# Kernel tuning notes

Measured on AMD Instinct MI355X. Metric: run time of the kernel, lower is better.

## Reference

```python
import jax, jax.numpy as jnp
import numpy as np

G = 128        # number of graphs
N = 512        # nodes per graph
F_IN = 128     # n_feat
H = 128        # agg_hidden
L = 5          # n_layer
FC = 128       # fc_hidden
C = 10         # n_class
E_HALF = 8192  # undirected edge pairs per graph (symmetrized -> 16384 directed)


def setup_inputs() -> dict:
    key = jax.random.key(0)
    ks = jax.random.split(key, 8)
    x = jax.random.normal(ks[0], (G * N, F_IN), dtype=jnp.float32)
    # per-graph random edges, offset into the block-diagonal node index space
    s = jax.random.randint(ks[1], (G, E_HALF), 0, N)
    d = jax.random.randint(ks[2], (G, E_HALF), 0, N)
    off = (jnp.arange(G) * N)[:, None]
    s = (s + off).reshape(-1)
    d = (d + off).reshape(-1)
    src = jnp.concatenate([s, d])  # symmetric adjacency (edges + reversed)
    dst = jnp.concatenate([d, s])
    eps = jnp.zeros((L,), jnp.float32)  # nn.Parameter(torch.zeros(n_layer))
    W = jax.random.normal(ks[3], (L, H, H), jnp.float32) / jnp.sqrt(H)
    b = jnp.zeros((L, H), jnp.float32)
    fc1_w = jax.random.normal(ks[4], (H, FC), jnp.float32) / jnp.sqrt(H)
    fc1_b = jnp.zeros((FC,), jnp.float32)
    fc2_w = jax.random.normal(ks[5], (FC, C), jnp.float32) / jnp.sqrt(FC)
    fc2_b = jnp.zeros((C,), jnp.float32)
    return {"x": x, "eps": eps, "W": W, "b": b,
            "fc1_w": fc1_w, "fc1_b": fc1_b, "fc2_w": fc2_w, "fc2_b": fc2_b,
            "src": src, "dst": dst}


def reference(x, eps, W, b, fc1_w, fc1_b, fc2_w, fc2_b, src, dst):
    n = x.shape[0]
    h = x
    for i in range(L):
        # sparse Adj @ h : gather along src, scatter-add to dst
        pooled = jax.ops.segment_sum(h[src], dst, num_segments=n)
        h = jax.nn.relu(((1.0 + eps[i]) * h + pooled) @ W[i] + b[i])
        # dropout p=0.0 / eval mode -> identity
    hg = h.reshape(G, N, -1).sum(axis=1)          # sum readout over nodes
    hg = jax.nn.relu(hg @ fc1_w + fc1_b)
    return jax.nn.softmax(hg @ fc2_w + fc2_b, axis=-1)
```

## Files before the change

### kernel.cpp

```cpp
#include <hip/hip_runtime.h>

#define NODES 65536
#define GNUM  128
#define NPG   512
#define FDIM  128

#define OFF_A   0u
#define OFF_WT  (16u<<20)
#define OFF_HTA (17u<<20)
#define OFF_HTB (33u<<20)

typedef short bf16x8 __attribute__((ext_vector_type(8)));
typedef float f32x4  __attribute__((ext_vector_type(4)));
typedef unsigned short u16;

#define GLB_AS __attribute__((address_space(1)))
#define LDS_AS __attribute__((address_space(3)))

static __device__ inline void gload16(const void* g, void* l) {
    __builtin_amdgcn_global_load_lds((const GLB_AS unsigned*)g,
                                     (LDS_AS unsigned*)l, 16, 0, 0);
}

static __device__ inline unsigned bf1(float x) {
    unsigned b = __float_as_uint(x);
    return (b + 0x7fffu + ((b >> 16) & 1u)) >> 16;
}
static __device__ inline unsigned pack_bf2(float x, float y) {
    return bf1(x) | (bf1(y) << 16);
}
static __device__ inline bf16x8 cvt8n(unsigned x) {
    union { bf16x8 v; unsigned u[4]; } r;
#pragma unroll
    for (int i = 0; i < 4; ++i) {
        float f0 = (float)((x >> (8 * i)) & 0xFu);
        float f1 = (float)((x >> (8 * i + 4)) & 0xFu);
        r.u[i] = (__float_as_uint(f0) >> 16) | (__float_as_uint(f1) & 0xffff0000u);
    }
    return r.v;
}

__global__ __launch_bounds__(256) void k_cvtT(const float* __restrict__ x,
                                              u16* __restrict__ hT) {
    __shared__ char Cs[128 * 144];
    int t = threadIdx.x;
    int m0 = blockIdx.x * 64;
    int g = m0 >> 9, ml0 = m0 & 511;
#pragma unroll
    for (int it = 0; it < 8; ++it) {
        int i = t + 256 * it;
        int nl = i >> 5, fq = i & 31;
        float4 v = *(const float4*)(x + (size_t)(m0 + nl) * FDIM + fq * 4);
        *(u16*)(Cs + (fq * 4 + 0) * 144 + nl * 2) = (u16)bf1(v.x);
        *(u16*)(Cs + (fq * 4 + 1) * 144 + nl * 2) = (u16)bf1(v.y);
        *(u16*)(Cs + (fq * 4 + 2) * 144 + nl * 2) = (u16)bf1(v.z);
        *(u16*)(Cs + (fq * 4 + 3) * 144 + nl * 2) = (u16)bf1(v.w);
    }
    __syncthreads();
    u16* hg = hT + (size_t)g * 65536 + ml0;
#pragma unroll
    for (int j = 0; j < 4; ++j) {
        int idx = t + 256 * j;
        int f = idx >> 3, piece = idx & 7;
        uint4 v = *(const uint4*)(Cs + f * 144 + piece * 16);
        *(uint4*)((char*)(hg + (size_t)f * 512) + piece * 16) = v;
    }
}

__global__ __launch_bounds__(256) void k_wt(const float* __restrict__ W,
                                            u16* __restrict__ wt) {
    int idx = blockIdx.x * 256 + threadIdx.x;
    int l = idx >> 14, r = idx & 16383;
    int n = r >> 7, k = r & 127;
    wt[idx] = (u16)bf1(W[(l << 14) + k * 128 + n]);
}

__global__ __launch_bounds__(1024) void k_adense(const int* __restrict__ src,
                                                 const int* __restrict__ dst,
                                                 unsigned* __restrict__ A4,
                                                 int halfE) {
    __shared__ uint4 cnt4[512 * 16];
    unsigned* cnt = (unsigned*)cnt4;
    int g = blockIdx.x;
    int t = threadIdx.x;
#pragma unroll
    for (int j = 0; j < 8; ++j) cnt4[t + 1024 * j] = make_uint4(0u, 0u, 0u, 0u);
    __syncthreads();
    int epg = halfE / GNUM;
#pragma unroll
    for (int r = 0; r < 2; ++r) {
        int base = r * halfE + g * epg;
        const int4* s4 = (const int4*)(src + base);
        const int4* d4 = (const int4*)(dst + base);
#pragma unroll
        for (int it = 0; it < 2; ++it) {
            int i = t + 1024 * it;
            int4 sv = s4[i], dv = d4[i];
            int s, d;
            s = sv.x & 511; d = dv.x & 511; atomicAdd(&cnt[d * 64 + (s >> 3)], 1u << ((s & 7) * 4));
            s = sv.y & 511; d = dv.y & 511; atomicAdd(&cnt[d * 64 + (s >> 3)], 1u << ((s & 7) * 4));
            s = sv.z & 511; d = dv.z & 511; atomicAdd(&cnt[d * 64 + (s >> 3)], 1u << ((s & 7) * 4));
            s = sv.w & 511; d = dv.w & 511; atomicAdd(&cnt[d * 64 + (s >> 3)], 1u << ((s & 7) * 4));
        }
    }
    __syncthreads();
    uint4* Ao = (uint4*)(A4 + (size_t)g * 512 * 64);
#pragma unroll
    for (int j = 0; j < 8; ++j) Ao[t + 1024 * j] = cnt4[t + 1024 * j];
}

__global__ __launch_bounds__(256, 2) void k_layer(const u16* __restrict__ hT,
                                                  u16* __restrict__ hTo,
                                                  const unsigned char* __restrict__ A,
                                                  const u16* __restrict__ wt,
                                                  const float* __restrict__ bias,
                                                  const float* __restrict__ eps) {
    __shared__ uint4 smem16[75776 / 16];
    char* smem = (char*)smem16;
    char* Ps = smem + 40960;
    int t = threadIdx.x;
    int w = t >> 6, lane = t & 63;
    int q = lane >> 4, ln = lane & 15;
    int g = blockIdx.x & 127, dq = blockIdx.x >> 7;
    const unsigned char* Ab = A + (size_t)g * (512 * 256) + (size_t)dq * 128 * 256;
    const u16* hb = hT + (size_t)g * 65536;

    int pA = t;
    int rowA = pA >> 1;
    const unsigned char* gA = Ab + rowA * 256 + (pA & 1) * 16;
    f32x4 acc[2][8];
#pragma unroll
    for (int mt = 0; mt < 2; ++mt)
#pragma unroll
        for (int nt = 0; nt < 8; ++nt) acc[mt][nt] = (f32x4){0.f, 0.f, 0.f, 0.f};

    gload16(gA, smem + pA * 16);
#pragma unroll
    for (int j = 0; j < 4; ++j) {
        int p = t + 256 * j; int f = p >> 3;
        gload16((const char*)hb + (size_t)f * 1024 + (((p & 7) ^ (f & 7)) << 4),
                smem + 8192 + p * 16);
    }
    __syncthreads();
    int rA0 = w * 32 + ln;
    for (int ch = 0; ch < 8; ++ch) {
        char* Asc = smem + (ch & 1) * 4096;
        char* Bsc = smem + 8192 + (ch & 1) * 16384;
        if (ch < 7) {
            char* Asn = smem + ((ch + 1) & 1) * 4096;
            char* Bsn = smem + 8192 + ((ch + 1) & 1) * 16384;
            gload16(gA + (ch + 1) * 32, Asn + pA * 16);
#pragma unroll
            for (int j = 0; j < 4; ++j) {
                int p = t + 256 * j; int f = p >> 3;
                gload16((const char*)hb + (size_t)f * 1024 + (ch + 1) * 128
                            + (((p & 7) ^ (f & 7)) << 4),
                        Bsn + p * 16);
            }
        }
#pragma unroll
        for (int kcL = 0; kcL < 2; ++kcL) {
            bf16x8 af0 = cvt8n(*(const unsigned*)(Asc + rA0 * 32 + kcL * 16 + q * 4));
            bf16x8 af1 = cvt8n(*(const unsigned*)(Asc + (rA0 + 16) * 32 + kcL * 16 + q * 4));
#pragma unroll
            for (int nt = 0; nt < 8; ++nt) {
                int f = nt * 16 + ln;
                int sB = f * 8 + ((kcL * 4 + q) ^ (f & 7));
                bf16x8 bf = *(const bf16x8*)(Bsc + sB * 16);
                acc[0][nt] = __builtin_amdgcn_mfma_f32_16x16x32_bf16(af0, bf, acc[0][nt], 0, 0, 0);
                acc[1][nt] = __builtin_amdgcn_mfma_f32_16x16x32_bf16(af1, bf, acc[1][nt], 0, 0, 0);
            }
        }
        __syncthreads();
    }
    float ep = 1.f + eps[0];
#pragma unroll
    for (int mt = 0; mt < 2; ++mt) {
        int rl0 = w * 32 + mt * 16 + q * 4;
        int mb0 = dq * 128 + rl0;
#pragma unroll
        for (int nt = 0; nt < 8; ++nt) {
            int f = nt * 16 + ln;
            uint2 sv = *(const uint2*)(hb + (size_t)f * 512 + mb0);
            float s0 = __uint_as_float(sv.x << 16);
            float s1 = __uint_as_float(sv.x & 0xffff0000u);
            float s2 = __uint_as_float(sv.y << 16);
            float s3 = __uint_as_float(sv.y & 0xffff0000u);
            f32x4 a = acc[mt][nt];
            *(u16*)(Ps + (rl0 + 0) * 272 + f * 2) = (u16)bf1(fmaf(ep, s0, a[0]));
            *(u16*)(Ps + (rl0 + 1) * 272 + f * 2) = (u16)bf1(fmaf(ep, s1, a[1]));
            *(u16*)(Ps + (rl0 + 2) * 272 + f * 2) = (u16)bf1(fmaf(ep, s2, a[2]));
            *(u16*)(Ps + (rl0 + 3) * 272 + f * 2) = (u16)bf1(fmaf(ep, s3, a[3]));
        }
    }
    __syncthreads();
    f32x4 acc2[2][8];
#pragma unroll
    for (int mt = 0; mt < 2; ++mt)
#pragma unroll
        for (int nt = 0; nt < 8; ++nt) acc2[mt][nt] = (f32x4){0.f, 0.f, 0.f, 0.f};
#pragma unroll
    for (int ks = 0; ks < 4; ++ks) {
        bf16x8 af0 = *(const bf16x8*)(Ps + rA0 * 272 + ks * 64 + q * 16);
        bf16x8 af1 = *(const bf16x8*)(Ps + (rA0 + 16) * 272 + ks * 64 + q * 16);
#pragma unroll
        for (int nt = 0; nt < 8; ++nt) {
            bf16x8 bf = *(const bf16x8*)(wt + (size_t)(nt * 16 + ln) * 128 + ks * 32 + q * 8);
            acc2[0][nt] = __builtin_amdgcn_mfma_f32_16x16x32_bf16(af0, bf, acc2[0][nt], 0, 0, 0);
            acc2[1][nt] = __builtin_amdgcn_mfma_f32_16x16x32_bf16(af1, bf, acc2[1][nt], 0, 0, 0);
        }
    }
    __syncthreads();
#pragma unroll
    for (int mt = 0; mt < 2; ++mt) {
        int rl0 = w * 32 + mt * 16 + q * 4;
#pragma unroll
        for (int nt = 0; nt < 8; ++nt) {
            int n = nt * 16 + ln;
            float bv = bias[n];
            f32x4 a = acc2[mt][nt];
            *(uint2*)(Ps + n * 272 + rl0 * 2) =
                make_uint2(pack_bf2(fmaxf(a[0] + bv, 0.f), fmaxf(a[1] + bv, 0.f)),
                           pack_bf2(fmaxf(a[2] + bv, 0.f), fmaxf(a[3] + bv, 0.f)));
        }
    }
    __syncthreads();
    u16* ho = hTo + (size_t)g * 65536 + dq * 128;
#pragma unroll
    for (int j = 0; j < 8; ++j) {
        int idx = t + 256 * j;
        int f = idx >> 4, piece = idx & 15;
        uint4 v = *(const uint4*)(Ps + f * 272 + piece * 16);
        *(uint4*)((char*)(ho + (size_t)f * 512) + piece * 16) = v;
    }
}

__global__ __launch_bounds__(128) void k_r(const u16* __restrict__ hT,
                                           const float* __restrict__ fc1w,
                                           const float* __restrict__ fc1b,
                                           const float* __restrict__ fc2w,
                                           const float* __restrict__ fc2b,
                                           float* __restrict__ out) {
    __shared__ float hg[128], z[128], lg[10];
    int g = blockIdx.x, t = threadIdx.x;
    const uint4* row = (const uint4*)(hT + (size_t)g * 65536 + (size_t)t * 512);
    float acc = 0.f;
#pragma unroll 4
    for (int i = 0; i < 64; ++i) {
        uint4 u = row[i];
        acc += __uint_as_float(u.x << 16) + __uint_as_float(u.x & 0xffff0000u);
        acc += __uint_as_float(u.y << 16) + __uint_as_float(u.y & 0xffff0000u);
        acc += __uint_as_float(u.z << 16) + __uint_as_float(u.z & 0xffff0000u);
        acc += __uint_as_float(u.w << 16) + __uint_as_float(u.w & 0xffff0000u);
    }
    hg[t] = acc;
    __syncthreads();
    float a1 = fc1b[t];
#pragma unroll 4
    for (int k = 0; k < 128; ++k) a1 = fmaf(hg[k], fc1w[k * 128 + t], a1);
    z[t] = fmaxf(a1, 0.f);
    __syncthreads();
    if (t < 10) {
        float l2 = fc2b[t];
        for (int k = 0; k < 128; ++k) l2 = fmaf(z[k], fc2w[k * 10 + t], l2);
        lg[t] = l2;
    }
    __syncthreads();
    if (t < 10) {
        float m = lg[0];
        for (int c = 1; c < 10; ++c) m = fmaxf(m, lg[c]);
        float ssum = 0.f;
        for (int c = 0; c < 10; ++c) ssum += expf(lg[c] - m);
        out[g * 10 + t] = expf(lg[t] - m) / ssum;
    }
}

extern "C" void kernel_launch(void* const* d_in, const int* in_sizes, int n_in,
                              void* d_out, int out_size, void* d_ws, size_t ws_size,
                              hipStream_t stream) {
    const float* x    = (const float*)d_in[0];
    const float* eps  = (const float*)d_in[1];
    const float* W    = (const float*)d_in[2];
    const float* b    = (const float*)d_in[3];
    const float* fc1w = (const float*)d_in[4];
    const float* fc1b = (const float*)d_in[5];
    const float* fc2w = (const float*)d_in[6];
    const float* fc2b = (const float*)d_in[7];
    const int*   src  = (const int*)d_in[8];
    const int*   dst  = (const int*)d_in[9];
    int E = in_sizes[8];
    int halfE = E >> 1;

    char* ws  = (char*)d_ws;
    unsigned char* Abuf = (unsigned char*)(ws + OFF_A);
    u16*  wtb = (u16*)(ws + OFF_WT);
    u16*  hta = (u16*)(ws + OFF_HTA);
    u16*  htb = (u16*)(ws + OFF_HTB);
    float* out = (float*)d_out;

    k_cvtT<<<NODES / 64, 256, 0, stream>>>(x, hta);
    k_wt<<<5 * 128 * 128 / 256, 256, 0, stream>>>(W, wtb);
    k_adense<<<GNUM, 1024, 0, stream>>>(src, dst, (unsigned*)Abuf, halfE);

    u16* cur = hta;
    u16* nxt = htb;
    for (int l = 0; l < 5; ++l) {
        k_layer<<<GNUM * 4, 256, 0, stream>>>(cur, nxt, Abuf,
                                              wtb + l * 128 * 128, b + l * 128, eps + l);
        u16* tmp = cur; cur = nxt; nxt = tmp;
    }
    k_r<<<GNUM, 128, 0, stream>>>(cur, fc1w, fc1b, fc2w, fc2b, out);
}
```

Measured before the change: 251.0 us.

## Triple-buffer adjacency and feature tiles with explicit vmcnt waits in layer kernel

Converts the double-buffered k-loop in the layer kernel into a three-stage ring buffer that prefetches two chunks ahead. It replaces __syncthreads with manual s_waitcnt vmcnt counts plus raw barriers, so that more global-to-LDS loads stay in flight while the MFMAs run. The output staging buffer now overlaps the ring buffer, which lowers total LDS use. The hand-set vmcnt values rely on an exact count of outstanding loads per thread, so a wrong count would cause data races.

```diff
diff --git a/kernel.cpp b/kernel.cpp
--- a/kernel.cpp
+++ b/kernel.cpp
@@ -115,9 +115,9 @@
                                                   const u16* __restrict__ wt,
                                                   const float* __restrict__ bias,
                                                   const float* __restrict__ eps) {
-    __shared__ uint4 smem16[75776 / 16];
+    __shared__ uint4 smem16[61440 / 16];
     char* smem = (char*)smem16;
-    char* Ps = smem + 40960;
+    char* Ps = smem + 12288;
     int t = threadIdx.x;
     int w = t >> 6, lane = t & 63;
     int q = lane >> 4, ln = lane & 15;
@@ -126,38 +126,46 @@
     const u16* hb = hT + (size_t)g * 65536;
 
     int pA = t;
-    int rowA = pA >> 1;
-    const unsigned char* gA = Ab + rowA * 256 + (pA & 1) * 16;
+    const unsigned char* gA = Ab + (pA >> 1) * 256 + (pA & 1) * 16;
     f32x4 acc[2][8];
 #pragma unroll
     for (int mt = 0; mt < 2; ++mt)
 #pragma unroll
         for (int nt = 0; nt < 8; ++nt) acc[mt][nt] = (f32x4){0.f, 0.f, 0.f, 0.f};
 
-    gload16(gA, smem + pA * 16);
-#pragma unroll
-    for (int j = 0; j < 4; ++j) {
-        int p = t + 256 * j; int f = p >> 3;
-        gload16((const char*)hb + (size_t)f * 1024 + (((p & 7) ^ (f & 7)) << 4),
-                smem + 8192 + p * 16);
-    }
-    __syncthreads();
+#pragma unroll
+    for (int c = 0; c < 2; ++c) {
+        gload16(gA + c * 32, smem + c * 4096 + pA * 16);
+#pragma unroll
+        for (int j = 0; j < 4; ++j) {
+            int p = t + 256 * j; int f = p >> 3;
+            gload16((const char*)hb + (size_t)f * 1024 + c * 128
+                        + (((p & 7) ^ (f & 7)) << 4),
+                    smem + 12288 + c * 16384 + p * 16);
+        }
+    }
     int rA0 = w * 32 + ln;
+#pragma unroll
     for (int ch = 0; ch < 8; ++ch) {
-        char* Asc = smem + (ch & 1) * 4096;
-        char* Bsc = smem + 8192 + (ch & 1) * 16384;
-        if (ch < 7) {
-            char* Asn = smem + ((ch + 1) & 1) * 4096;
-            char* Bsn = smem + 8192 + ((ch + 1) & 1) * 16384;
-            gload16(gA + (ch + 1) * 32, Asn + pA * 16);
+        char* Asc = smem + (ch % 3) * 4096;
+        char* Bsc = smem + 12288 + (ch % 3) * 16384;
+        if (ch + 2 < 8) {
+            int cn = ch + 2;
+            char* Asn = smem + (cn % 3) * 4096;
+            char* Bsn = smem + 12288 + (cn % 3) * 16384;
+            gload16(gA + cn * 32, Asn + pA * 16);
 #pragma unroll
             for (int j = 0; j < 4; ++j) {
                 int p = t + 256 * j; int f = p >> 3;
-                gload16((const char*)hb + (size_t)f * 1024 + (ch + 1) * 128
+                gload16((const char*)hb + (size_t)f * 1024 + cn * 128
                             + (((p & 7) ^ (f & 7)) << 4),
                         Bsn + p * 16);
             }
         }
+        if (ch < 6)      asm volatile("s_waitcnt vmcnt(10)" ::: "memory");
+        else if (ch < 7) asm volatile("s_waitcnt vmcnt(5)" ::: "memory");
+        else             asm volatile("s_waitcnt vmcnt(0)" ::: "memory");
+        __builtin_amdgcn_s_barrier();
 #pragma unroll
         for (int kcL = 0; kcL < 2; ++kcL) {
             bf16x8 af0 = cvt8n(*(const unsigned*)(Asc + rA0 * 32 + kcL * 16 + q * 4));
@@ -171,7 +179,7 @@
                 acc[1][nt] = __builtin_amdgcn_mfma_f32_16x16x32_bf16(af1, bf, acc[1][nt], 0, 0, 0);
             }
         }
-        __syncthreads();
+        __builtin_amdgcn_s_barrier();
     }
     float ep = 1.f + eps[0];
 #pragma unroll
```

After: 245.6 us. 2.1% less time.

## Fuse all GIN layers and readout into one persistent per-graph kernel

Applied to the files above, without the earlier changes.

Replaces the five per-layer launches and the readout launch with a single kernel that runs one 1024-thread block per graph. Each block keeps the graph's transposed bf16 node features resident in 128 KB of LDS across all layers, so they no longer round-trip through global memory between layers. The dense-W matmul is serialized over four quarters of the nodes to fit in LDS scratch. The readout and MLP run in the same kernel, and the x and W conversion kernels are merged into one launch. The trade-off is only 128 blocks (one per graph, one block per CU), plus quarter-serialized phases with many barriers, which may underuse the GPU compared with 512 blocks per layer.

```diff
diff --git a/kernel.cpp b/kernel.cpp
--- a/kernel.cpp
+++ b/kernel.cpp
@@ -1,6 +1,5 @@
 #include <hip/hip_runtime.h>
 
-#define NODES 65536
 #define GNUM  128
 #define NPG   512
 #define FDIM  128
@@ -8,7 +7,6 @@
 #define OFF_A   0u
 #define OFF_WT  (16u<<20)
 #define OFF_HTA (17u<<20)
-#define OFF_HTB (33u<<20)
 
 typedef short bf16x8 __attribute__((ext_vector_type(8)));
 typedef float f32x4  __attribute__((ext_vector_type(4)));
@@ -40,11 +38,21 @@
     return r.v;
 }
 
-__global__ __launch_bounds__(256) void k_cvtT(const float* __restrict__ x,
-                                              u16* __restrict__ hT) {
+__global__ __launch_bounds__(256) void k_prep(const float* __restrict__ x,
+                                              u16* __restrict__ hT,
+                                              const float* __restrict__ W,
+                                              u16* __restrict__ wt) {
     __shared__ char Cs[128 * 144];
     int t = threadIdx.x;
-    int m0 = blockIdx.x * 64;
+    int bid = blockIdx.x;
+    if (bid >= 1024) {
+        int idx = (bid - 1024) * 256 + t;
+        int l = idx >> 14, r = idx & 16383;
+        int n = r >> 7, k = r & 127;
+        wt[idx] = (u16)bf1(W[(l << 14) + k * 128 + n]);
+        return;
+    }
+    int m0 = bid * 64;
     int g = m0 >> 9, ml0 = m0 & 511;
 #pragma unroll
     for (int it = 0; it < 8; ++it) {
@@ -65,14 +73,6 @@
         uint4 v = *(const uint4*)(Cs + f * 144 + piece * 16);
         *(uint4*)((char*)(hg + (size_t)f * 512) + piece * 16) = v;
     }
-}
-
-__global__ __launch_bounds__(256) void k_wt(const float* __restrict__ W,
-                                            u16* __restrict__ wt) {
-    int idx = blockIdx.x * 256 + threadIdx.x;
-    int l = idx >> 14, r = idx & 16383;
-    int n = r >> 7, k = r & 127;
-    wt[idx] = (u16)bf1(W[(l << 14) + k * 128 + n]);
 }
 
 __global__ __launch_bounds__(1024) void k_adense(const int* __restrict__ src,
@@ -109,160 +109,162 @@
     for (int j = 0; j < 8; ++j) Ao[t + 1024 * j] = cnt4[t + 1024 * j];
 }
 
-__global__ __launch_bounds__(256, 2) void k_layer(const u16* __restrict__ hT,
-                                                  u16* __restrict__ hTo,
-                                                  const unsigned char* __restrict__ A,
-                                                  const u16* __restrict__ wt,
-                                                  const float* __restrict__ bias,
-                                                  const float* __restrict__ eps) {
-    __shared__ uint4 smem16[75776 / 16];
-    char* smem = (char*)smem16;
-    char* Ps = smem + 40960;
+__global__ __launch_bounds__(1024) void k_gin(
+        const u16* __restrict__ hT,
+        const unsigned char* __restrict__ A,
+        const u16* __restrict__ wt,
+        const float* __restrict__ bias,
+        const float* __restrict__ eps,
+        const float* __restrict__ fc1w, const float* __restrict__ fc1b,
+        const float* __restrict__ fc2w, const float* __restrict__ fc2b,
+        float* __restrict__ out) {
+    __shared__ uint4 smem16[163840 / 16];
+    char* hTl = (char*)smem16;
+    char* scr = (char*)smem16 + 131072;
     int t = threadIdx.x;
     int w = t >> 6, lane = t & 63;
     int q = lane >> 4, ln = lane & 15;
-    int g = blockIdx.x & 127, dq = blockIdx.x >> 7;
-    const unsigned char* Ab = A + (size_t)g * (512 * 256) + (size_t)dq * 128 * 256;
-    const u16* hb = hT + (size_t)g * 65536;
-
-    int pA = t;
-    int rowA = pA >> 1;
-    const unsigned char* gA = Ab + rowA * 256 + (pA & 1) * 16;
-    f32x4 acc[2][8];
-#pragma unroll
-    for (int mt = 0; mt < 2; ++mt)
-#pragma unroll
-        for (int nt = 0; nt < 8; ++nt) acc[mt][nt] = (f32x4){0.f, 0.f, 0.f, 0.f};
-
-    gload16(gA, smem + pA * 16);
-#pragma unroll
-    for (int j = 0; j < 4; ++j) {
-        int p = t + 256 * j; int f = p >> 3;
-        gload16((const char*)hb + (size_t)f * 1024 + (((p & 7) ^ (f & 7)) << 4),
-                smem + 8192 + p * 16);
-    }
-    __syncthreads();
+    int g = blockIdx.x;
+    const unsigned char* Ab = A + (size_t)g * 131072;
+    const u16* hgb = hT + (size_t)g * 65536;
     int rA0 = w * 32 + ln;
-    for (int ch = 0; ch < 8; ++ch) {
-        char* Asc = smem + (ch & 1) * 4096;
-        char* Bsc = smem + 8192 + (ch & 1) * 16384;
-        if (ch < 7) {
-            char* Asn = smem + ((ch + 1) & 1) * 4096;
-            char* Bsn = smem + 8192 + ((ch + 1) & 1) * 16384;
-            gload16(gA + (ch + 1) * 32, Asn + pA * 16);
-#pragma unroll
-            for (int j = 0; j < 4; ++j) {
-                int p = t + 256 * j; int f = p >> 3;
-                gload16((const char*)hb + (size_t)f * 1024 + (ch + 1) * 128
-                            + (((p & 7) ^ (f & 7)) << 4),
-                        Bsn + p * 16);
+
+#pragma unroll
+    for (int j = 0; j < 8; ++j) {
+        int p = t + 1024 * j;
+        int f = p >> 6, bb = p & 63;
+        gload16((const char*)hgb + (size_t)f * 1024 + ((bb ^ (f & 7)) << 4),
+                hTl + p * 16);
+    }
+    const unsigned char* gA = Ab + (t >> 1) * 256 + (t & 1) * 16;
+
+    for (int l = 0; l < 5; ++l) {
+        const u16* wl = wt + l * 16384;
+        float ep = 1.f + eps[l];
+        gload16(gA, scr + t * 16);
+        f32x4 acc[2][8];
+#pragma unroll
+        for (int mt = 0; mt < 2; ++mt)
+#pragma unroll
+            for (int nt = 0; nt < 8; ++nt) acc[mt][nt] = (f32x4){0.f, 0.f, 0.f, 0.f};
+#pragma unroll
+        for (int ch = 0; ch < 8; ++ch) {
+            char* Asc = scr + (ch & 1) * 16384;
+            if (ch < 7) {
+                gload16(gA + (ch + 1) * 32, scr + ((ch + 1) & 1) * 16384 + t * 16);
+                asm volatile("s_waitcnt vmcnt(1)" ::: "memory");
+            } else {
+                asm volatile("s_waitcnt vmcnt(0)" ::: "memory");
             }
+            __builtin_amdgcn_s_barrier();
+#pragma unroll
+            for (int kcL = 0; kcL < 2; ++kcL) {
+                bf16x8 af0 = cvt8n(*(const unsigned*)(Asc + rA0 * 32 + kcL * 16 + q * 4));
+                bf16x8 af1 = cvt8n(*(const unsigned*)(Asc + (rA0 + 16) * 32 + kcL * 16 + q * 4));
+#pragma unroll
+                for (int nt = 0; nt < 8; ++nt) {
+                    int f = nt * 16 + ln;
+                    int bb = (ch * 8 + ((kcL * 4 + q) ^ (f & 7))) << 4;
+                    bf16x8 bf = *(const bf16x8*)(hTl + f * 1024 + bb);
+                    acc[0][nt] = __builtin_amdgcn_mfma_f32_16x16x32_bf16(af0, bf, acc[0][nt], 0, 0, 0);
+                    acc[1][nt] = __builtin_amdgcn_mfma_f32_16x16x32_bf16(af1, bf, acc[1][nt], 0, 0, 0);
+                }
+            }
+            __builtin_amdgcn_s_barrier();
         }
-#pragma unroll
-        for (int kcL = 0; kcL < 2; ++kcL) {
-            bf16x8 af0 = cvt8n(*(const unsigned*)(Asc + rA0 * 32 + kcL * 16 + q * 4));
-            bf16x8 af1 = cvt8n(*(const unsigned*)(Asc + (rA0 + 16) * 32 + kcL * 16 + q * 4));
-#pragma unroll
-            for (int nt = 0; nt < 8; ++nt) {
-                int f = nt * 16 + ln;
-                int sB = f * 8 + ((kcL * 4 + q) ^ (f & 7));
-                bf16x8 bf = *(const bf16x8*)(Bsc + sB * 16);
-                acc[0][nt] = __builtin_amdgcn_mfma_f32_16x16x32_bf16(af0, bf, acc[0][nt], 0, 0, 0);
-                acc[1][nt] = __builtin_amdgcn_mfma_f32_16x16x32_bf16(af1, bf, acc[1][nt], 0, 0, 0);
+        for (int qp = 0; qp < 4; ++qp) {
+            if ((w >> 2) == qp) {
+#pragma unroll
+                for (int mt = 0; mt < 2; ++mt) {
+                    int rl0 = (w & 3) * 32 + mt * 16 + q * 4;
+                    int node0 = qp * 128 + rl0;
+#pragma unroll
+                    for (int nt = 0; nt < 8; ++nt) {
+                        int f = nt * 16 + ln;
+                        const char* sp = hTl + f * 1024
+                            + (((node0 >> 3) ^ (f & 7)) << 4) + (node0 & 7) * 2;
+                        uint2 sv = *(const uint2*)sp;
+                        float s0 = __uint_as_float(sv.x << 16);
+                        float s1 = __uint_as_float(sv.x & 0xffff0000u);
+                        float s2 = __uint_as_float(sv.y << 16);
+                        float s3 = __uint_as_float(sv.y & 0xffff0000u);
+                        f32x4 a = acc[mt][nt];
+                        int r0 = rl0 + 0, r1 = rl0 + 1, r2 = rl0 + 2, r3 = rl0 + 3;
+                        *(u16*)(scr + r0 * 256 + ((f * 2) ^ ((r0 & 7) << 4))) = (u16)bf1(fmaf(ep, s0, a[0]));
+                        *(u16*)(scr + r1 * 256 + ((f * 2) ^ ((r1 & 7) << 4))) = (u16)bf1(fmaf(ep, s1, a[1]));
+                        *(u16*)(scr + r2 * 256 + ((f * 2) ^ ((r2 & 7) << 4))) = (u16)bf1(fmaf(ep, s2, a[2]));
+                        *(u16*)(scr + r3 * 256 + ((f * 2) ^ ((r3 & 7) << 4))) = (u16)bf1(fmaf(ep, s3, a[3]));
+                    }
+                }
             }
+            __syncthreads();
+            if ((w >> 2) == qp) {
+                f32x4 acc2[2][8];
+#pragma unroll
+                for (int mt = 0; mt < 2; ++mt)
+#pragma unroll
+                    for (int nt = 0; nt < 8; ++nt) acc2[mt][nt] = (f32x4){0.f, 0.f, 0.f, 0.f};
+                int r0 = (w & 3) * 32 + ln;
+                int xr = (r0 & 7) << 4;
+#pragma unroll
+                for (int ks = 0; ks < 4; ++ks) {
+                    bf16x8 af0 = *(const bf16x8*)(scr + r0 * 256 + ((ks * 64 + q * 16) ^ xr));
+                    bf16x8 af1 = *(const bf16x8*)(scr + (r0 + 16) * 256 + ((ks * 64 + q * 16) ^ xr));
+#pragma unroll
+                    for (int nt = 0; nt < 8; ++nt) {
+                        bf16x8 bf = *(const bf16x8*)(wl + (size_t)(nt * 16 + ln) * 128 + ks * 32 + q * 8);
+                        acc2[0][nt] = __builtin_amdgcn_mfma_f32_16x16x32_bf16(af0, bf, acc2[0][nt], 0, 0, 0);
+                        acc2[1][nt] = __builtin_amdgcn_mfma_f32_16x16x32_bf16(af1, bf, acc2[1][nt], 0, 0, 0);
+                    }
+                }
+#pragma unroll
+                for (int mt = 0; mt < 2; ++mt) {
+                    int rl0 = (w & 3) * 32 + mt * 16 + q * 4;
+                    int node0 = qp * 128 + rl0;
+#pragma unroll
+                    for (int nt = 0; nt < 8; ++nt) {
+                        int n = nt * 16 + ln;
+                        float bv = bias[l * 128 + n];
+                        f32x4 a = acc2[mt][nt];
+                        char* op = hTl + n * 1024
+                            + (((node0 >> 3) ^ (n & 7)) << 4) + (node0 & 7) * 2;
+                        *(uint2*)op =
+                            make_uint2(pack_bf2(fmaxf(a[0] + bv, 0.f), fmaxf(a[1] + bv, 0.f)),
+                                       pack_bf2(fmaxf(a[2] + bv, 0.f), fmaxf(a[3] + bv, 0.f)));
+                    }
+                }
+            }
+            __syncthreads();
         }
-        __syncthreads();
-    }
-    float ep = 1.f + eps[0];
-#pragma unroll
-    for (int mt = 0; mt < 2; ++mt) {
-        int rl0 = w * 32 + mt * 16 + q * 4;
-        int mb0 = dq * 128 + rl0;
-#pragma unroll
-        for (int nt = 0; nt < 8; ++nt) {
-            int f = nt * 16 + ln;
-            uint2 sv = *(const uint2*)(hb + (size_t)f * 512 + mb0);
-            float s0 = __uint_as_float(sv.x << 16);
-            float s1 = __uint_as_float(sv.x & 0xffff0000u);
-            float s2 = __uint_as_float(sv.y << 16);
-            float s3 = __uint_as_float(sv.y & 0xffff0000u);
-            f32x4 a = acc[mt][nt];
-            *(u16*)(Ps + (rl0 + 0) * 272 + f * 2) = (u16)bf1(fmaf(ep, s0, a[0]));
-            *(u16*)(Ps + (rl0 + 1) * 272 + f * 2) = (u16)bf1(fmaf(ep, s1, a[1]));
-            *(u16*)(Ps + (rl0 + 2) * 272 + f * 2) = (u16)bf1(fmaf(ep, s2, a[2]));
-            *(u16*)(Ps + (rl0 + 3) * 272 + f * 2) = (u16)bf1(fmaf(ep, s3, a[3]));
+    }
+    float* hg = (float*)scr;
+    float* zz = hg + 128;
+    float* lg = zz + 128;
+    if (t < 128) {
+        float acc = 0.f;
+        const char* row = hTl + (size_t)t * 1024;
+#pragma unroll 4
+        for (int i = 0; i < 64; ++i) {
+            int bb = (i + (t & 63)) & 63;
+            uint4 u = *(const uint4*)(row + bb * 16);
+            acc += __uint_as_float(u.x << 16) + __uint_as_float(u.x & 0xffff0000u);
+            acc += __uint_as_float(u.y << 16) + __uint_as_float(u.y & 0xffff0000u);
+            acc += __uint_as_float(u.z << 16) + __uint_as_float(u.z & 0xffff0000u);
+            acc += __uint_as_float(u.w << 16) + __uint_as_float(u.w & 0xffff0000u);
         }
-    }
-    __syncthreads();
-    f32x4 acc2[2][8];
-#pragma unroll
-    for (int mt = 0; mt < 2; ++mt)
-#pragma unroll
-        for (int nt = 0; nt < 8; ++nt) acc2[mt][nt] = (f32x4){0.f, 0.f, 0.f, 0.f};
-#pragma unroll
-    for (int ks = 0; ks < 4; ++ks) {
-        bf16x8 af0 = *(const bf16x8*)(Ps + rA0 * 272 + ks * 64 + q * 16);
-        bf16x8 af1 = *(const bf16x8*)(Ps + (rA0 + 16) * 272 + ks * 64 + q * 16);
-#pragma unroll
-        for (int nt = 0; nt < 8; ++nt) {
-            bf16x8 bf = *(const bf16x8*)(wt + (size_t)(nt * 16 + ln) * 128 + ks * 32 + q * 8);
-            acc2[0][nt] = __builtin_amdgcn_mfma_f32_16x16x32_bf16(af0, bf, acc2[0][nt], 0, 0, 0);
-            acc2[1][nt] = __builtin_amdgcn_mfma_f32_16x16x32_bf16(af1, bf, acc2[1][nt], 0, 0, 0);
-        }
-    }
-    __syncthreads();
-#pragma unroll
-    for (int mt = 0; mt < 2; ++mt) {
-        int rl0 = w * 32 + mt * 16 + q * 4;
-#pragma unroll
-        for (int nt = 0; nt < 8; ++nt) {
-            int n = nt * 16 + ln;
-            float bv = bias[n];
-            f32x4 a = acc2[mt][nt];
-            *(uint2*)(Ps + n * 272 + rl0 * 2) =
-                make_uint2(pack_bf2(fmaxf(a[0] + bv, 0.f), fmaxf(a[1] + bv, 0.f)),
-                           pack_bf2(fmaxf(a[2] + bv, 0.f), fmaxf(a[3] + bv, 0.f)));
-        }
-    }
-    __syncthreads();
-    u16* ho = hTo + (size_t)g * 65536 + dq * 128;
-#pragma unroll
-    for (int j = 0; j < 8; ++j) {
-        int idx = t + 256 * j;
-        int f = idx >> 4, piece = idx & 15;
-        uint4 v = *(const uint4*)(Ps + f * 272 + piece * 16);
-        *(uint4*)((char*)(ho + (size_t)f * 512) + piece * 16) = v;
-    }
-}
-
-__global__ __launch_bounds__(128) void k_r(const u16* __restrict__ hT,
-                                           const float* __restrict__ fc1w,
-                                           const float* __restrict__ fc1b,
-                                           const float* __restrict__ fc2w,
-                                           const float* __restrict__ fc2b,
-                                           float* __restrict__ out) {
-    __shared__ float hg[128], z[128], lg[10];
-    int g = blockIdx.x, t = threadIdx.x;
-    const uint4* row = (const uint4*)(hT + (size_t)g * 65536 + (size_t)t * 512);
-    float acc = 0.f;
+        hg[t] = acc;
+    }
+    __syncthreads();
+    if (t < 128) {
+        float a1 = fc1b[t];
 #pragma unroll 4
-    for (int i = 0; i < 64; ++i) {
-        uint4 u = row[i];
-        acc += __uint_as_float(u.x << 16) + __uint_as_float(u.x & 0xffff0000u);
-        acc += __uint_as_float(u.y << 16) + __uint_as_float(u.y & 0xffff0000u);
-        acc += __uint_as_float(u.z << 16) + __uint_as_float(u.z & 0xffff0000u);
-        acc += __uint_as_float(u.w << 16) + __uint_as_float(u.w & 0xffff0000u);
-    }
-    hg[t] = acc;
-    __syncthreads();
-    float a1 = fc1b[t];
-#pragma unroll 4
-    for (int k = 0; k < 128; ++k) a1 = fmaf(hg[k], fc1w[k * 128 + t], a1);
-    z[t] = fmaxf(a1, 0.f);
+        for (int k = 0; k < 128; ++k) a1 = fmaf(hg[k], fc1w[k * 128 + t], a1);
+        zz[t] = fmaxf(a1, 0.f);
+    }
     __syncthreads();
     if (t < 10) {
         float l2 = fc2b[t];
-        for (int k = 0; k < 128; ++k) l2 = fmaf(z[k], fc2w[k * 10 + t], l2);
+        for (int k = 0; k < 128; ++k) l2 = fmaf(zz[k], fc2w[k * 10 + t], l2);
         lg[t] = l2;
     }
     __syncthreads();
@@ -295,19 +297,10 @@
     unsigned char* Abuf = (unsigned char*)(ws + OFF_A);
     u16*  wtb = (u16*)(ws + OFF_WT);
     u16*  hta = (u16*)(ws + OFF_HTA);
-    u16*  htb = (u16*)(ws + OFF_HTB);
     float* out = (float*)d_out;
 
-    k_cvtT<<<NODES / 64, 256, 0, stream>>>(x, hta);
-    k_wt<<<5 * 128 * 128 / 256, 256, 0, stream>>>(W, wtb);
+    k_prep<<<1344, 256, 0, stream>>>(x, hta, W, wtb);
     k_adense<<<GNUM, 1024, 0, stream>>>(src, dst, (unsigned*)Abuf, halfE);
-
-    u16* cur = hta;
-    u16* nxt = htb;
-    for (int l = 0; l < 5; ++l) {
-        k_layer<<<GNUM * 4, 256, 0, stream>>>(cur, nxt, Abuf,
-                                              wtb + l * 128 * 128, b + l * 128, eps + l);
-        u16* tmp = cur; cur = nxt; nxt = tmp;
-    }
-    k_r<<<GNUM, 128, 0, stream>>>(cur, fc1w, fc1b, fc2w, fc2b, out);
-}
+    k_gin<<<GNUM, 1024, 0, stream>>>(hta, Abuf, wtb, b, eps,
+                                     fc1w, fc1b, fc2w, fc2b, out);
+}
```

New measurement: 869.2 us. 3.46x slower.

## Split layer kernel into 64-row blocks, hold adjacency in registers, fuse prep kernels

Applied to the files above, without the earlier changes.

Each layer block now covers 64 destination rows instead of 128, so the grid doubles to 1024 blocks. The four waves are split as 2 row halves by 2 feature halves. The adjacency tile is preloaded into registers rather than staged through LDS, which shrinks shared memory from about 74KB to 32KB and allows 4 blocks per CU. The per-chunk sync becomes an explicit vmcnt wait plus barrier. The feature transpose and weight transpose kernels are merged into one launch. In exchange, every block now loads the full 128-feature h slab for only half as many output rows, doubling that traffic, and register pressure rises from the 32-entry adjacency array.

```diff
diff --git a/kernel.cpp b/kernel.cpp
--- a/kernel.cpp
+++ b/kernel.cpp
@@ -1,6 +1,5 @@
 #include <hip/hip_runtime.h>
 
-#define NODES 65536
 #define GNUM  128
 #define NPG   512
 #define FDIM  128
@@ -40,11 +39,21 @@
     return r.v;
 }
 
-__global__ __launch_bounds__(256) void k_cvtT(const float* __restrict__ x,
-                                              u16* __restrict__ hT) {
+__global__ __launch_bounds__(256) void k_prep(const float* __restrict__ x,
+                                              u16* __restrict__ hT,
+                                              const float* __restrict__ W,
+                                              u16* __restrict__ wt) {
     __shared__ char Cs[128 * 144];
     int t = threadIdx.x;
-    int m0 = blockIdx.x * 64;
+    int bid = blockIdx.x;
+    if (bid >= 1024) {
+        int idx = (bid - 1024) * 256 + t;
+        int l = idx >> 14, r = idx & 16383;
+        int n = r >> 7, k = r & 127;
+        wt[idx] = (u16)bf1(W[(l << 14) + k * 128 + n]);
+        return;
+    }
+    int m0 = bid * 64;
     int g = m0 >> 9, ml0 = m0 & 511;
 #pragma unroll
     for (int it = 0; it < 8; ++it) {
@@ -67,14 +76,6 @@
     }
 }
 
-__global__ __launch_bounds__(256) void k_wt(const float* __restrict__ W,
-                                            u16* __restrict__ wt) {
-    int idx = blockIdx.x * 256 + threadIdx.x;
-    int l = idx >> 14, r = idx & 16383;
-    int n = r >> 7, k = r & 127;
-    wt[idx] = (u16)bf1(W[(l << 14) + k * 128 + n]);
-}
-
 __global__ __launch_bounds__(1024) void k_adense(const int* __restrict__ src,
                                                  const int* __restrict__ dst,
                                                  unsigned* __restrict__ A4,
@@ -109,47 +110,51 @@
     for (int j = 0; j < 8; ++j) Ao[t + 1024 * j] = cnt4[t + 1024 * j];
 }
 
-__global__ __launch_bounds__(256, 2) void k_layer(const u16* __restrict__ hT,
+__global__ __launch_bounds__(256, 4) void k_layer(const u16* __restrict__ hT,
                                                   u16* __restrict__ hTo,
                                                   const unsigned char* __restrict__ A,
                                                   const u16* __restrict__ wt,
                                                   const float* __restrict__ bias,
                                                   const float* __restrict__ eps) {
-    __shared__ uint4 smem16[75776 / 16];
+    __shared__ uint4 smem16[32768 / 16];
     char* smem = (char*)smem16;
-    char* Ps = smem + 40960;
+    char* Ps = smem;
     int t = threadIdx.x;
     int w = t >> 6, lane = t & 63;
     int q = lane >> 4, ln = lane & 15;
     int g = blockIdx.x & 127, dq = blockIdx.x >> 7;
-    const unsigned char* Ab = A + (size_t)g * (512 * 256) + (size_t)dq * 128 * 256;
+    const unsigned char* Ab = A + (size_t)g * 131072 + (size_t)dq * 64 * 256;
     const u16* hb = hT + (size_t)g * 65536;
-
-    int pA = t;
-    int rowA = pA >> 1;
-    const unsigned char* gA = Ab + rowA * 256 + (pA & 1) * 16;
-    f32x4 acc[2][8];
+    int rA0 = (w & 1) * 32 + ln;
+    int fh0 = (w >> 1) * 64;
+
+    unsigned aA[32];
+#pragma unroll
+    for (int ch = 0; ch < 8; ++ch)
+#pragma unroll
+        for (int kcL = 0; kcL < 2; ++kcL)
+#pragma unroll
+            for (int h = 0; h < 2; ++h)
+                aA[ch * 4 + kcL * 2 + h] = *(const unsigned*)
+                    (Ab + (size_t)(rA0 + h * 16) * 256 + ch * 32 + kcL * 16 + q * 4);
+
+    f32x4 acc[2][4];
 #pragma unroll
     for (int mt = 0; mt < 2; ++mt)
 #pragma unroll
-        for (int nt = 0; nt < 8; ++nt) acc[mt][nt] = (f32x4){0.f, 0.f, 0.f, 0.f};
-
-    gload16(gA, smem + pA * 16);
+        for (int nt = 0; nt < 4; ++nt) acc[mt][nt] = (f32x4){0.f, 0.f, 0.f, 0.f};
+
 #pragma unroll
     for (int j = 0; j < 4; ++j) {
         int p = t + 256 * j; int f = p >> 3;
         gload16((const char*)hb + (size_t)f * 1024 + (((p & 7) ^ (f & 7)) << 4),
-                smem + 8192 + p * 16);
-    }
-    __syncthreads();
-    int rA0 = w * 32 + ln;
+                smem + p * 16);
+    }
+#pragma unroll
     for (int ch = 0; ch < 8; ++ch) {
-        char* Asc = smem + (ch & 1) * 4096;
-        char* Bsc = smem + 8192 + (ch & 1) * 16384;
+        char* Bsc = smem + (ch & 1) * 16384;
         if (ch < 7) {
-            char* Asn = smem + ((ch + 1) & 1) * 4096;
-            char* Bsn = smem + 8192 + ((ch + 1) & 1) * 16384;
-            gload16(gA + (ch + 1) * 32, Asn + pA * 16);
+            char* Bsn = smem + ((ch + 1) & 1) * 16384;
 #pragma unroll
             for (int j = 0; j < 4; ++j) {
                 int p = t + 256 * j; int f = p >> 3;
@@ -157,30 +162,34 @@
                             + (((p & 7) ^ (f & 7)) << 4),
                         Bsn + p * 16);
             }
-        }
+            asm volatile("s_waitcnt vmcnt(4)" ::: "memory");
+        } else {
+            asm volatile("s_waitcnt vmcnt(0)" ::: "memory");
+        }
+        __builtin_amdgcn_s_barrier();
 #pragma unroll
         for (int kcL = 0; kcL < 2; ++kcL) {
-            bf16x8 af0 = cvt8n(*(const unsigned*)(Asc + rA0 * 32 + kcL * 16 + q * 4));
-            bf16x8 af1 = cvt8n(*(const unsigned*)(Asc + (rA0 + 16) * 32 + kcL * 16 + q * 4));
-#pragma unroll
-            for (int nt = 0; nt < 8; ++nt) {
-                int f = nt * 16 + ln;
+            bf16x8 af0 = cvt8n(aA[ch * 4 + kcL * 2 + 0]);
+            bf16x8 af1 = cvt8n(aA[ch * 4 + kcL * 2 + 1]);
+#pragma unroll
+            for (int nt = 0; nt < 4; ++nt) {
+                int f = fh0 + nt * 16 + ln;
                 int sB = f * 8 + ((kcL * 4 + q) ^ (f & 7));
                 bf16x8 bf = *(const bf16x8*)(Bsc + sB * 16);
                 acc[0][nt] = __builtin_amdgcn_mfma_f32_16x16x32_bf16(af0, bf, acc[0][nt], 0, 0, 0);
                 acc[1][nt] = __builtin_amdgcn_mfma_f32_16x16x32_bf16(af1, bf, acc[1][nt], 0, 0, 0);
             }
         }
-        __syncthreads();
+        __builtin_amdgcn_s_barrier();
     }
     float ep = 1.f + eps[0];
 #pragma unroll
     for (int mt = 0; mt < 2; ++mt) {
-        int rl0 = w * 32 + mt * 16 + q * 4;
-        int mb0 = dq * 128 + rl0;
-#pragma unroll
-        for (int nt = 0; nt < 8; ++nt) {
-            int f = nt * 16 + ln;
+        int rl0 = (w & 1) * 32 + mt * 16 + q * 4;
+        int mb0 = dq * 64 + rl0;
+#pragma unroll
+        for (int nt = 0; nt < 4; ++nt) {
+            int f = fh0 + nt * 16 + ln;
             uint2 sv = *(const uint2*)(hb + (size_t)f * 512 + mb0);
             float s0 = __uint_as_float(sv.x << 16);
             float s1 = __uint_as_float(sv.x & 0xffff0000u);
@@ -194,18 +203,19 @@
         }
     }
     __syncthreads();
-    f32x4 acc2[2][8];
+    f32x4 acc2[2][4];
 #pragma unroll
     for (int mt = 0; mt < 2; ++mt)
 #pragma unroll
-        for (int nt = 0; nt < 8; ++nt) acc2[mt][nt] = (f32x4){0.f, 0.f, 0.f, 0.f};
+        for (int nt = 0; nt < 4; ++nt) acc2[mt][nt] = (f32x4){0.f, 0.f, 0.f, 0.f};
 #pragma unroll
     for (int ks = 0; ks < 4; ++ks) {
         bf16x8 af0 = *(const bf16x8*)(Ps + rA0 * 272 + ks * 64 + q * 16);
         bf16x8 af1 = *(const bf16x8*)(Ps + (rA0 + 16) * 272 + ks * 64 + q * 16);
 #pragma unroll
-        for (int nt = 0; nt < 8; ++nt) {
-            bf16x8 bf = *(const bf16x8*)(wt + (size_t)(nt * 16 + ln) * 128 + ks * 32 + q * 8);
+        for (int nt = 0; nt < 4; ++nt) {
+            int n = fh0 + nt * 16 + ln;
+            bf16x8 bf = *(const bf16x8*)(wt + (size_t)n * 128 + ks * 32 + q * 8);
             acc2[0][nt] = __builtin_amdgcn_mfma_f32_16x16x32_bf16(af0, bf, acc2[0][nt], 0, 0, 0);
             acc2[1][nt] = __builtin_amdgcn_mfma_f32_16x16x32_bf16(af1, bf, acc2[1][nt], 0, 0, 0);
         }
@@ -213,24 +223,24 @@
     __syncthreads();
 #pragma unroll
     for (int mt = 0; mt < 2; ++mt) {
-        int rl0 = w * 32 + mt * 16 + q * 4;
-#pragma unroll
-        for (int nt = 0; nt < 8; ++nt) {
-            int n = nt * 16 + ln;
+        int rl0 = (w & 1) * 32 + mt * 16 + q * 4;
+#pragma unroll
+        for (int nt = 0; nt < 4; ++nt) {
+            int n = fh0 + nt * 16 + ln;
             float bv = bias[n];
             f32x4 a = acc2[mt][nt];
-            *(uint2*)(Ps + n * 272 + rl0 * 2) =
+            *(uint2*)(Ps + n * 144 + rl0 * 2) =
                 make_uint2(pack_bf2(fmaxf(a[0] + bv, 0.f), fmaxf(a[1] + bv, 0.f)),
                            pack_bf2(fmaxf(a[2] + bv, 0.f), fmaxf(a[3] + bv, 0.f)));
         }
     }
     __syncthreads();
-    u16* ho = hTo + (size_t)g * 65536 + dq * 128;
-#pragma unroll
-    for (int j = 0; j < 8; ++j) {
+    u16* ho = hTo + (size_t)g * 65536 + dq * 64;
+#pragma unroll
+    for (int j = 0; j < 4; ++j) {
         int idx = t + 256 * j;
-        int f = idx >> 4, piece = idx & 15;
-        uint4 v = *(const uint4*)(Ps + f * 272 + piece * 16);
+        int f = idx >> 3, piece = idx & 7;
+        uint4 v = *(const uint4*)(Ps + f * 144 + piece * 16);
         *(uint4*)((char*)(ho + (size_t)f * 512) + piece * 16) = v;
     }
 }
@@ -298,14 +308,13 @@
     u16*  htb = (u16*)(ws + OFF_HTB);
     float* out = (float*)d_out;
 
-    k_cvtT<<<NODES / 64, 256, 0, stream>>>(x, hta);
-    k_wt<<<5 * 128 * 128 / 256, 256, 0, stream>>>(W, wtb);
+    k_prep<<<1344, 256, 0, stream>>>(x, hta, W, wtb);
     k_adense<<<GNUM, 1024, 0, stream>>>(src, dst, (unsigned*)Abuf, halfE);
 
     u16* cur = hta;
     u16* nxt = htb;
     for (int l = 0; l < 5; ++l) {
-        k_layer<<<GNUM * 4, 256, 0, stream>>>(cur, nxt, Abuf,
+        k_layer<<<GNUM * 8, 256, 0, stream>>>(cur, nxt, Abuf,
                                               wtb + l * 128 * 128, b + l * 128, eps + l);
         u16* tmp = cur; cur = nxt; nxt = tmp;
     }
```

Measured after the change: 291.7 us. 16.2% more time.
